# Optimization experiments

Hardware: AMD Instinct MI355X
Metric: run time of the kernel (lower is better)

The kernel has to match this reference:

```python
import jax, jax.numpy as jnp
import numpy as np

B, DIM, OC, H, W, HEADS = 4, 128, 128, 128, 128, 8
L = H * W
_BN_INV = 1.0 / (1.0 + 1e-5) ** 0.5  # eval-mode BN: running_mean=0, running_var=1


def conv2d(x, w, b=None, groups=1, pad=0):
    y = jax.lax.conv_general_dilated(
        x, w, (1, 1), [(pad, pad), (pad, pad)],
        dimension_numbers=('NCHW', 'OIHW', 'NCHW'),
        feature_group_count=groups)
    if b is not None:
        y = y + b[None, :, None, None]
    return y


def bn(x, g, b):
    return x * (g * _BN_INV)[None, :, None, None] + b[None, :, None, None]


def ln(x, g, b, eps=1e-5):
    m = jnp.mean(x, -1, keepdims=True)
    v = jnp.mean((x - m) ** 2, -1, keepdims=True)
    return (x - m) * jax.lax.rsqrt(v + eps) * g + b


def rope_tables(h, w, c, base=10000.0):
    k_max = c // 4
    theta = 1.0 / base ** (np.arange(k_max, dtype=np.float32) / k_max)
    gi, gj = np.meshgrid(np.arange(h, dtype=np.float32),
                         np.arange(w, dtype=np.float32), indexing='ij')
    ang = np.concatenate([gi[..., None] * theta, gj[..., None] * theta], -1)  # (h,w,c//2)
    return jnp.asarray(np.cos(ang)), jnp.asarray(np.sin(ang))


def apply_rope(x, cs, sn):  # x: (b,h,w,c); consecutive pairs = (re, im)
    xr, xi = x[..., 0::2], x[..., 1::2]
    return jnp.stack([cs * xr - sn * xi, sn * xr + cs * xi], -1).reshape(x.shape)


def linear_attn(x, qk_w, qk_b, lepe_w, lepe_b, h, w):
    b, n, c = x.shape
    hd = c // HEADS
    qk = x @ qk_w.T + qk_b
    q = jax.nn.elu(qk[..., :c]) + 1.0
    k = jax.nn.elu(qk[..., c:]) + 1.0
    cs, sn = rope_tables(h, w, c)

    def heads(t):  # (b,n,c) -> (b,HEADS,n,hd)
        return t.reshape(b, n, HEADS, hd).transpose(0, 2, 1, 3)

    q_r = heads(apply_rope(q.reshape(b, h, w, c), cs, sn).reshape(b, n, c))
    k_r = heads(apply_rope(k.reshape(b, h, w, c), cs, sn).reshape(b, n, c))
    qh, kh, vh = heads(q), heads(k), heads(x)
    k_mean = jnp.mean(kh, axis=2, keepdims=True)                      # (b,Hd,1,hd)
    z = 1.0 / (jnp.einsum('bhnd,bhmd->bhnm', qh, k_mean) + 1e-6)      # (b,Hd,n,1)
    s = n ** -0.5
    kv = jnp.einsum('bhnd,bhne->bhde', k_r * s, vh * s)               # (b,Hd,hd,hd)
    out = jnp.einsum('bhnd,bhde->bhne', q_r, kv) * z
    out = out.transpose(0, 2, 1, 3).reshape(b, n, c)
    v_img = x.reshape(b, h, w, c).transpose(0, 3, 1, 2)
    lepe = conv2d(v_img, lepe_w, lepe_b, groups=c, pad=1)
    return out + lepe.transpose(0, 2, 3, 1).reshape(b, n, c)


def fmt_block(xb, fw1, fb1, f_g, f_be, fw2, fb2, n_g, n_be):
    t = jnp.fft.fft2(xb)                                              # (B,C,H,W) complex
    wgt = jax.nn.relu(bn(conv2d(t.real, fw1, fb1), f_g, f_be))
    wgt = jax.nn.sigmoid(conv2d(wgt, fw2, fb2))
    f = jnp.abs(jnp.fft.ifft2(wgt * t))
    f = jax.nn.relu(bn(f, n_g, n_be))
    return f.reshape(f.shape[0], f.shape[1], -1).transpose(0, 2, 1)   # (B,L,C)


def _forward(x, c1_w, c1_b, c1_g, c1_be, cpe1_w, cpe1_b,
             fw1, fb1, f_g, f_be, fw2, fb2, nbn_g, nbn_be,
             ln1_g, ln1_b, d3w1, d3b1, d3w2, d5w1, d5b1, d5w2,
             ap_w, ap_b, ip2_w, ip2_b, dwc2_w, dwc2_b,
             qk_w, qk_b, lepe_w, lepe_b, op_w, op_b,
             cpe2_w, cpe2_b, ln2_g, ln2_b,
             ffn_w1, ffn_b1, ffn_w2, ffn_b2, po_w,
             red_w, red_b, red_g, red_be):
    Bb, C, Hh, Ww = x.shape
    Ll = Hh * Ww
    to_img = lambda t: t.reshape(Bb, Hh, Ww, C).transpose(0, 3, 1, 2)   # (B,L,C)->(B,C,H,W)
    to_seq = lambda t: t.transpose(0, 2, 3, 1).reshape(Bb, Ll, -1)       # (B,C,H,W)->(B,L,C)

    x_0 = jax.nn.relu(bn(conv2d(x, c1_w, c1_b), c1_g, c1_be))           # (B,OC,H,W)
    xt = to_seq(x + conv2d(x, cpe1_w, cpe1_b, groups=C, pad=1))
    shortcut = xt
    fmt1 = fmt_block(to_img(xt), fw1, fb1, f_g, f_be, fw2, fb2, nbn_g, nbn_be)

    x_s = ln(xt, ln1_g, ln1_b)
    xs_img = to_img(x_s)
    x_s3 = conv2d(conv2d(xs_img, d3w1, d3b1), d3w2, None, groups=C // 2, pad=1)
    x_s5 = conv2d(conv2d(xs_img, d5w1, d5b1), d5w2, None, groups=C // 2, pad=2)
    act_res = jax.nn.silu(to_seq(conv2d(xs_img, ap_w, ap_b)))

    def branch(t):  # (B,C/2,H,W) -> (B,L,C/2)
        t = conv2d(t, ip2_w, ip2_b)
        t = jax.nn.silu(conv2d(t, dwc2_w, dwc2_b, groups=C // 2, pad=1))
        return to_seq(t)

    a3 = linear_attn(branch(x_s3), qk_w, qk_b, lepe_w, lepe_b, Hh, Ww)
    a5 = linear_attn(branch(x_s5), qk_w, qk_b, lepe_w, lepe_b, Hh, Ww)
    xs = jnp.concatenate([a3, a5], -1)
    xs = to_seq(conv2d(to_img(xs * act_res), op_w, op_b))

    xt = shortcut + xs + fmt1
    xt = xt + to_seq(conv2d(to_img(xt), cpe2_w, cpe2_b, groups=C, pad=1))
    fmt2 = fmt_block(to_img(xt), fw1, fb1, f_g, f_be, fw2, fb2, nbn_g, nbn_be)
    h2 = ln(xt, ln2_g, ln2_b)
    ffn = jax.nn.gelu(h2 @ ffn_w1.T + ffn_b1, approximate=False) @ ffn_w2.T + ffn_b2
    xt = xt + ffn + fmt2

    xo = conv2d(to_img(xt), po_w)                                        # (B,OC,H,W)
    cat = jnp.concatenate([x_0, xo], 1)
    return jax.nn.relu(bn(conv2d(cat, red_w, red_b), red_g, red_be)) + x_0


def setup_inputs():
    key = jax.random.key(0)
    it = iter(jax.random.split(key, 64))

    def w(shape, s=0.05):
        return jax.random.normal(next(it), shape, jnp.float32) * s

    d, oc = DIM, OC
    ones = lambda n: jnp.ones((n,), jnp.float32)
    zeros = lambda n: jnp.zeros((n,), jnp.float32)
    return {
        'x': jax.random.normal(next(it), (B, d, H, W), jnp.float32),
        'c1_w': w((oc, d, 1, 1)), 'c1_b': w((oc,), 0.01), 'c1_g': ones(oc), 'c1_be': zeros(oc),
        'cpe1_w': w((d, 1, 3, 3)), 'cpe1_b': w((d,), 0.01),
        'fw1': w((d // 16, d, 1, 1)), 'fb1': w((d // 16,), 0.01),
        'f_g': ones(d // 16), 'f_be': zeros(d // 16),
        'fw2': w((d, d // 16, 1, 1)), 'fb2': w((d,), 0.01),
        'nbn_g': ones(d), 'nbn_be': zeros(d),
        'ln1_g': ones(d), 'ln1_b': zeros(d),
        'd3w1': w((d, d, 1, 1)), 'd3b1': w((d,), 0.01), 'd3w2': w((d // 2, 2, 3, 3)),
        'd5w1': w((d, d, 1, 1)), 'd5b1': w((d,), 0.01), 'd5w2': w((d // 2, 2, 5, 5)),
        'ap_w': w((d, d, 1, 1)), 'ap_b': w((d,), 0.01),
        'ip2_w': w((d // 2, d // 2, 1, 1)), 'ip2_b': w((d // 2,), 0.01),
        'dwc2_w': w((d // 2, 1, 3, 3)), 'dwc2_b': w((d // 2,), 0.01),
        'qk_w': w((d, d // 2)), 'qk_b': w((d,), 0.01),
        'lepe_w': w((d // 2, 1, 3, 3)), 'lepe_b': w((d // 2,), 0.01),
        'op_w': w((d, d, 1, 1)), 'op_b': w((d,), 0.01),
        'cpe2_w': w((d, 1, 3, 3)), 'cpe2_b': w((d,), 0.01),
        'ln2_g': ones(d), 'ln2_b': zeros(d),
        'ffn_w1': w((4, d)), 'ffn_b1': w((4,), 0.01),
        'ffn_w2': w((d, 4)), 'ffn_b2': w((d,), 0.01),
        'po_w': w((oc, d, 1, 1)),
        'red_w': w((oc, 2 * oc, 1, 1)), 'red_b': w((oc,), 0.01),
        'red_g': ones(oc), 'red_be': zeros(oc),
    }


def reference(x, c1_w, c1_b, c1_g, c1_be, cpe1_w, cpe1_b,
              fw1, fb1, f_g, f_be, fw2, fb2, nbn_g, nbn_be,
              ln1_g, ln1_b, d3w1, d3b1, d3w2, d5w1, d5b1, d5w2,
              ap_w, ap_b, ip2_w, ip2_b, dwc2_w, dwc2_b,
              qk_w, qk_b, lepe_w, lepe_b, op_w, op_b,
              cpe2_w, cpe2_b, ln2_g, ln2_b,
              ffn_w1, ffn_b1, ffn_w2, ffn_b2, po_w,
              red_w, red_b, red_g, red_be):
    return _forward(x, c1_w, c1_b, c1_g, c1_be, cpe1_w, cpe1_b,
                    fw1, fb1, f_g, f_be, fw2, fb2, nbn_g, nbn_be,
                    ln1_g, ln1_b, d3w1, d3b1, d3w2, d5w1, d5b1, d5w2,
                    ap_w, ap_b, ip2_w, ip2_b, dwc2_w, dwc2_b,
                    qk_w, qk_b, lepe_w, lepe_b, op_w, op_b,
                    cpe2_w, cpe2_b, ln2_g, ln2_b,
                    ffn_w1, ffn_b1, ffn_w2, ffn_b2, po_w,
                    red_w, red_b, red_g, red_be)
```

## Files before the change

kernel.cpp:

```cpp
#include <hip/hip_runtime.h>
#include <math.h>

typedef unsigned short bf16_t;
typedef __attribute__((ext_vector_type(8))) short short8;
typedef __attribute__((ext_vector_type(4))) float f32x4;

#define B_ 4
#define C_ 128
#define H_ 128
#define W_ 128
#define L_ (H_*W_)
#define NS  ((size_t)B_*L_*C_)
#define NH  ((size_t)B_*L_*64)
#define NSP ((size_t)L_*C_)
#define PI_F 3.14159265358979323846f
#define BN_INV 0.9999950000374997f
#define THETA_SC 0.8304820237218406f
#define TOTW 157148
#define W16SHIFT 107548

__device__ __forceinline__ float ldf(bf16_t v){ return __uint_as_float(((unsigned)v)<<16); }
__device__ __forceinline__ bf16_t f2b(float f){
  unsigned u = __float_as_uint(f);
  u += 0x7fffu + ((u>>16)&1u);
  return (bf16_t)(u>>16);
}

#define WGSZ ((size_t)B_*8*L_)
#define ACCSZ 2304
#define CWSZ 157184
#define CW16SZF 78592
#define WSF (6*NS + 3*NH + WGSZ + ACCSZ + CWSZ + CW16SZF + 16)
__device__ float g_ws[WSF];

__global__ void k_probe(const bf16_t* __restrict__ xb, int* __restrict__ flag){
  __shared__ int vote;
  if (threadIdx.x == 0) vote = 0;
  __syncthreads();
  int bad = 0;
  for (int i = threadIdx.x; i < 2048; i += 256) {
    float v = ldf(xb[2*i]);
    if (!(fabsf(v) < 1e6f)) bad = 1;
  }
  if (bad) atomicOr(&vote, 1);
  __syncthreads();
  if (threadIdx.x == 0) *flag = vote;
}

struct P47 { const void* p[47]; };
__device__ __constant__ int c_wsz[47] = {
  16384,128,128,128,1152,128,1024,8,8,8,1024,128,128,128,128,128,
  16384,128,1152,16384,128,3200,16384,128,4096,64,576,64,8192,128,
  576,64,16384,128,1152,128,128,128,512,4,512,128,16384,32768,128,128,128};

__global__ __launch_bounds__(256) void k_cvt(P47 ps, const int* __restrict__ flagp,
                                             float* __restrict__ dst){
  int g = blockIdx.x*256 + threadIdx.x;
  if (g >= TOTW) return;
  int fl = *flagp;
  int idx = 0, off = g;
  while (off >= c_wsz[idx]) { off -= c_wsz[idx]; idx++; }
  const void* s = ps.p[idx];
  dst[g] = fl ? ((const float*)s)[off] : ldf(((const bf16_t*)s)[off]);
}

__global__ __launch_bounds__(256) void k_cvt16(const float* __restrict__ src, bf16_t* __restrict__ dst){
  int g = blockIdx.x*256 + threadIdx.x;
  if (g >= TOTW) return;
  dst[g + (g >= W16SHIFT ? 4 : 0)] = f2b(src[g]);
}

__global__ void k_zero(float* p, int n){
  int i = blockIdx.x*256 + threadIdx.x;
  if (i < n) p[i] = 0.f;
}

__device__ __forceinline__ void tw_fwd(int lane, float* tc, float* ts) {
  sincosf(-PI_F * (float)lane * (1.f/64.f), &ts[0], &tc[0]);
  int i = 1;
  #pragma unroll
  for (int m = 32; m >= 1; m >>= 1, i++) {
    int k = lane & (m-1);
    sincosf(-PI_F * (float)k / (float)m, &ts[i], &tc[i]);
  }
}
__device__ __forceinline__ void tw_inv(int lane, float* tc, float* ts) {
  int i = 0;
  #pragma unroll
  for (int m = 1; m <= 32; m <<= 1, i++) {
    int k = lane & (m-1);
    sincosf(PI_F * (float)k / (float)m, &ts[i], &tc[i]);
  }
  sincosf(PI_F * (float)lane * (1.f/64.f), &ts[6], &tc[6]);
}

__device__ __forceinline__ void fft128_fwd(float& lor, float& loi, float& hir, float& hii,
                                           int lane, const float* tc, const float* ts) {
  {
    float s = ts[0], c = tc[0];
    float ar = lor, ai = loi;
    float dr = ar - hir, di = ai - hii;
    lor = ar + hir; loi = ai + hii;
    hir = dr*c - di*s; hii = dr*s + di*c;
  }
  int i = 1;
  #pragma unroll
  for (int m = 32; m >= 1; m >>= 1, i++) {
    float s = ts[i], c = tc[i];
    bool up = (lane & m) != 0;
    {
      float orr = __shfl_xor(lor, m), oii = __shfl_xor(loi, m);
      float sr = lor + orr, si = loi + oii;
      float dr = orr - lor, di = oii - loi;
      float tr = dr*c - di*s, ti = dr*s + di*c;
      lor = up ? tr : sr; loi = up ? ti : si;
    }
    {
      float orr = __shfl_xor(hir, m), oii = __shfl_xor(hii, m);
      float sr = hir + orr, si = hii + oii;
      float dr = orr - hir, di = oii - hii;
      float tr = dr*c - di*s, ti = dr*s + di*c;
      hir = up ? tr : sr; hii = up ? ti : si;
    }
  }
}

__device__ __forceinline__ void fft128_inv(float& lor, float& loi, float& hir, float& hii,
                                           int lane, const float* tc, const float* ts) {
  int i = 0;
  #pragma unroll
  for (int m = 1; m <= 32; m <<= 1, i++) {
    float s = ts[i], c = tc[i];
    bool up = (lane & m) != 0;
    {
      float orr = __shfl_xor(lor, m), oii = __shfl_xor(loi, m);
      float qr = orr*c - oii*s, qi = orr*s + oii*c;
      float lo_r = lor + qr, lo_i = loi + qi;
      float mr = lor*c - loi*s, mi = lor*s + loi*c;
      float up_r = orr - mr, up_i = oii - mi;
      lor = up ? up_r : lo_r; loi = up ? up_i : lo_i;
    }
    {
      float orr = __shfl_xor(hir, m), oii = __shfl_xor(hii, m);
      float qr = orr*c - oii*s, qi = orr*s + oii*c;
      float lo_r = hir + qr, lo_i = hii + qi;
      float mr = hir*c - hii*s, mi = hir*s + hii*c;
      float up_r = orr - mr, up_i = oii - mi;
      hir = up ? up_r : lo_r; hii = up ? up_i : lo_i;
    }
  }
  {
    float s = ts[6], c = tc[6];
    float qr = hir*c - hii*s, qi = hir*s + hii*c;
    float pr = lor, pi = loi;
    lor = pr + qr; loi = pi + qi;
    hir = pr - qr; hii = pi - qi;
  }
}

__global__ __launch_bounds__(256) void k_fft_row_fwd_seq(
    const float* __restrict__ in, float* __restrict__ re, float* __restrict__ im) {
  __shared__ float T[64*130];
  int tid = threadIdx.x;
  int bid = blockIdx.x;
  int ch = (bid & 1) * 64;
  int h  = (bid >> 1) & 127;
  int b  = bid >> 8;
  const float* ip = in + ((size_t)b*L_ + (size_t)h*128)*128 + ch;
  #pragma unroll
  for (int it = 0; it < 8; it++) {
    int idx = it*256 + tid;
    int c4 = (idx & 15)*4, w = idx >> 4;
    float4 v = *(const float4*)(ip + (size_t)w*128 + c4);
    T[(c4+0)*130 + w] = v.x;
    T[(c4+1)*130 + w] = v.y;
    T[(c4+2)*130 + w] = v.z;
    T[(c4+3)*130 + w] = v.w;
  }
  __syncthreads();
  int lane = tid & 63, wv = tid >> 6;
  float tc[7], ts[7];
  tw_fwd(lane, tc, ts);
  size_t obase = (size_t)(b*128 + ch)*L_ + (size_t)h*128;
  for (int i = 0; i < 16; i++) {
    int cc = wv*16 + i;
    float lor = T[cc*130 + lane], loi = 0.f;
    float hir = T[cc*130 + 64 + lane], hii = 0.f;
    fft128_fwd(lor, loi, hir, hii, lane, tc, ts);
    size_t o = obase + (size_t)cc*L_;
    re[o + lane] = lor;      im[o + lane] = loi;
    re[o + lane + 64] = hir; im[o + lane + 64] = hii;
  }
}

__global__ __launch_bounds__(256) void k_fft_col_fwd(float* __restrict__ re, float* __restrict__ im) {
  __shared__ float Lre[128][33];
  __shared__ float Lim[128][33];
  int tid = threadIdx.x;
  size_t img = blockIdx.x >> 2;
  int w0 = (blockIdx.x & 3) * 32;
  float* rp = re + img * (size_t)L_ + w0;
  float* ip = im + img * (size_t)L_ + w0;
  for (int i = tid; i < 4096; i += 256) {
    int h = i >> 5, wl = i & 31;
    Lre[h][wl] = rp[(size_t)h*W_ + wl];
    Lim[h][wl] = ip[(size_t)h*W_ + wl];
  }
  __syncthreads();
  int lane = tid & 63, wv = tid >> 6;
  float tc[7], ts[7];
  tw_fwd(lane, tc, ts);
  for (int i = 0; i < 8; i++) {
    int col = wv*8 + i;
    float lor = Lre[lane][col], loi = Lim[lane][col];
    float hir = Lre[lane+64][col], hii = Lim[lane+64][col];
    fft128_fwd(lor, loi, hir, hii, lane, tc, ts);
    Lre[lane][col]=lor; Lim[lane][col]=loi;
    Lre[lane+64][col]=hir; Lim[lane+64][col]=hii;
  }
  __syncthreads();
  for (int i = tid; i < 4096; i += 256) {
    int h = i >> 5, wl = i & 31;
    rp[(size_t)h*W_ + wl] = Lre[h][wl];
    ip[(size_t)h*W_ + wl] = Lim[h][wl];
  }
}

__global__ __launch_bounds__(256) void k_fft_col_inv_scaled(
    float* __restrict__ re, float* __restrict__ im,
    const float* __restrict__ wg1, const float* __restrict__ fw2,
    const float* __restrict__ fb2) {
  __shared__ float Lre[128][33];
  __shared__ float Lim[128][33];
  __shared__ float w2r[8];
  int tid = threadIdx.x;
  size_t img = blockIdx.x >> 2;
  int c = (int)(img & 127);
  int b = (int)(img >> 7);
  int w0 = (blockIdx.x & 3) * 32;
  if (tid < 8) w2r[tid] = fw2[c*8 + tid];
  float b2 = fb2[c];
  float* rp = re + img * (size_t)L_ + w0;
  float* ip = im + img * (size_t)L_ + w0;
  const float* wgp = wg1 + (size_t)b*8*L_ + w0;
  __syncthreads();
  for (int i = tid; i < 4096; i += 256) {
    int h = i >> 5, wl = i & 31;
    size_t p = (size_t)h*W_ + wl;
    float a = b2;
    #pragma unroll
    for (int o = 0; o < 8; o++) a += w2r[o] * wgp[(size_t)o*L_ + p];
    float wgt = 1.f/(1.f+expf(-a));
    Lre[h][wl] = rp[p] * wgt;
    Lim[h][wl] = ip[p] * wgt;
  }
  __syncthreads();
  int lane = tid & 63, wv = tid >> 6;
  float tc[7], ts[7];
  tw_inv(lane, tc, ts);
  for (int i = 0; i < 8; i++) {
    int col = wv*8 + i;
    float lor = Lre[lane][col], loi = Lim[lane][col];
    float hir = Lre[lane+64][col], hii = Lim[lane+64][col];
    fft128_inv(lor, loi, hir, hii, lane, tc, ts);
    Lre[lane][col]=lor*(1.f/128.f); Lim[lane][col]=loi*(1.f/128.f);
    Lre[lane+64][col]=hir*(1.f/128.f); Lim[lane+64][col]=hii*(1.f/128.f);
  }
  __syncthreads();
  for (int i = tid; i < 4096; i += 256) {
    int h = i >> 5, wl = i & 31;
    rp[(size_t)h*W_ + wl] = Lre[h][wl];
    ip[(size_t)h*W_ + wl] = Lim[h][wl];
  }
}

__global__ __launch_bounds__(256) void k_fft_row_inv_abs_seq(
    const float* __restrict__ re, const float* __restrict__ im,
    const float* __restrict__ ng, const float* __restrict__ nbe,
    const float* __restrict__ add1, const float* __restrict__ add2,
    float* __restrict__ out) {
  __shared__ float T[64*130];
  int tid = threadIdx.x;
  int bid = blockIdx.x;
  int ch = (bid & 1) * 64;
  int h  = (bid >> 1) & 127;
  int b  = bid >> 8;
  int lane = tid & 63, wv = tid >> 6;
  float tc[7], ts[7];
  tw_inv(lane, tc, ts);
  size_t ibase = (size_t)(b*128 + ch)*L_ + (size_t)h*128;
  for (int i = 0; i < 16; i++) {
    int cc = wv*16 + i;
    size_t o = ibase + (size_t)cc*L_;
    float lor = re[o + lane], loi = im[o + lane];
    float hir = re[o + lane + 64], hii = im[o + lane + 64];
    fft128_inv(lor, loi, hir, hii, lane, tc, ts);
    float sg = ng[ch+cc]*BN_INV, sb = nbe[ch+cc];
    T[cc*130 + lane]      = fmaxf(sqrtf(lor*lor+loi*loi)*(1.f/128.f)*sg + sb, 0.f);
    T[cc*130 + 64 + lane] = fmaxf(sqrtf(hir*hir+hii*hii)*(1.f/128.f)*sg + sb, 0.f);
  }
  __syncthreads();
  size_t sb0 = ((size_t)b*L_ + (size_t)h*128)*128 + ch;
  #pragma unroll
  for (int it = 0; it < 8; it++) {
    int idx = it*256 + tid;
    int c4 = (idx & 15)*4, w = idx >> 4;
    size_t off = sb0 + (size_t)w*128 + c4;
    float4 v;
    v.x = T[(c4+0)*130 + w];
    v.y = T[(c4+1)*130 + w];
    v.z = T[(c4+2)*130 + w];
    v.w = T[(c4+3)*130 + w];
    float4 x1 = *(const float4*)(add1 + off);
    float4 x2 = *(const float4*)(add2 + off);
    v.x += x1.x + x2.x; v.y += x1.y + x2.y;
    v.z += x1.z + x2.z; v.w += x1.w + x2.w;
    *(float4*)(out + off) = v;
  }
}

__global__ __launch_bounds__(256) void k_freq1(const float* __restrict__ tre,
    const float* __restrict__ fw1, const float* __restrict__ fb1,
    const float* __restrict__ fg, const float* __restrict__ fbe,
    float* __restrict__ wg1) {
  __shared__ float w1s[1024];
  int tid = threadIdx.x;
  for (int i = tid; i < 1024; i += 256) w1s[i] = fw1[i];
  __syncthreads();
  size_t g = (size_t)blockIdx.x*256 + tid;
  int p = (int)(g & (L_-1));
  int b = (int)(g >> 14);
  const float* tp = tre + (size_t)b*128*L_ + p;
  float acc[8];
  #pragma unroll
  for (int o = 0; o < 8; o++) acc[o] = 0.f;
  for (int c = 0; c < 128; c++) {
    float v = tp[(size_t)c*L_];
    #pragma unroll
    for (int o = 0; o < 8; o++) acc[o] += w1s[o*128+c]*v;
  }
  size_t ob = (size_t)b*8*L_ + p;
  #pragma unroll
  for (int o = 0; o < 8; o++) {
    float v = (acc[o] + fb1[o]) * (fg[o]*BN_INV) + fbe[o];
    wg1[ob + (size_t)o*L_] = fmaxf(v, 0.f);
  }
}

template<bool DUAL>
__global__ void k_p2s(const void* __restrict__ src, float* __restrict__ dst,
                      const float* __restrict__ add1, const float* __restrict__ add2,
                      const int* __restrict__ flagp) {
  __shared__ float tile[32][33];
  int fl = DUAL ? *flagp : 1;
  int b = blockIdx.z;
  int p0 = blockIdx.x*32, c0 = blockIdx.y*32;
  int tx = threadIdx.x, ty = threadIdx.y;
  size_t base_in = (size_t)b*NSP;
  #pragma unroll
  for (int k = 0; k < 4; k++) {
    size_t off = base_in + (size_t)(c0+ty+8*k)*L_ + p0 + tx;
    float v;
    if (DUAL && !fl) v = ldf(((const bf16_t*)src)[off]);
    else             v = ((const float*)src)[off];
    tile[ty+8*k][tx] = v;
  }
  __syncthreads();
  size_t base = (size_t)b*NSP;
  #pragma unroll
  for (int k = 0; k < 4; k++) {
    size_t idx = base + (size_t)(p0+ty+8*k)*C_ + c0 + tx;
    float v = tile[tx][ty+8*k];
    if (add1) v += add1[idx];
    if (add2) v += add2[idx];
    dst[idx] = v;
  }
}

template<int CC, int MODE>
__global__ __launch_bounds__(256) void k_dw3(const float* __restrict__ in,
    const float* __restrict__ w, const float* __restrict__ bias,
    float* __restrict__ out) {
  __shared__ float wl[9*CC];
  int tid = threadIdx.x;
  for (int i = tid; i < 9*CC; i += 256) {
    int tap = i / CC, ch = i % CC;
    wl[i] = w[ch*9 + tap];
  }
  __syncthreads();
  size_t g = (size_t)blockIdx.x*256 + tid;
  int c = (int)(g & (CC-1));
  float wr[9];
  #pragma unroll
  for (int t = 0; t < 9; t++) wr[t] = wl[t*CC + c];
  size_t s = g / CC;
  int w0 = (int)(s & 31) * 4;
  int hp = (int)((s >> 5) & 127);
  int b  = (int)(s >> 12);
  const float* ip = in + (size_t)b*L_*CC + c;
  float bi = bias[c];
  float a0 = bi, a1 = bi, a2 = bi, a3 = bi;
  #pragma unroll
  for (int dh = -1; dh <= 1; dh++) {
    int h2 = hp + dh;
    if ((unsigned)h2 >= 128u) continue;
    const float* rp = ip + (size_t)h2*W_*CC;
    float px[6];
    #pragma unroll
    for (int x = 0; x < 6; x++) {
      int w2 = w0 - 1 + x;
      px[x] = ((unsigned)w2 < 128u) ? rp[(size_t)w2*CC] : 0.f;
    }
    #pragma unroll
    for (int dw = 0; dw < 3; dw++) {
      float f = wr[(dh+1)*3 + dw];
      a0 += f*px[dw];   a1 += f*px[dw+1];
      a2 += f*px[dw+2]; a3 += f*px[dw+3];
    }
  }
  size_t tb = (size_t)b*L_ + (size_t)hp*W_ + w0;
  if (MODE == 0) {
    out[(tb+0)*CC + c] = in[(tb+0)*CC + c] + a0;
    out[(tb+1)*CC + c] = in[(tb+1)*CC + c] + a1;
    out[(tb+2)*CC + c] = in[(tb+2)*CC + c] + a2;
    out[(tb+3)*CC + c] = in[(tb+3)*CC + c] + a3;
  } else {
    out[(tb+0)*CC + c] = a0 / (1.f + expf(-a0));
    out[(tb+1)*CC + c] = a1 / (1.f + expf(-a1));
    out[(tb+2)*CC + c] = a2 / (1.f + expf(-a2));
    out[(tb+3)*CC + c] = a3 / (1.f + expf(-a3));
  }
}

template<int K>
__global__ __launch_bounds__(256) void k_gconv(const float* __restrict__ in,
    const float* __restrict__ w, float* __restrict__ out) {
  __shared__ float wl[K*K*128];
  int tid = threadIdx.x;
  for (int i = tid; i < 128*K*K; i += 256) {
    int tap = i >> 7, ch = i & 127;
    wl[i] = w[ch*(K*K) + tap];
  }
  __syncthreads();
  size_t g = (size_t)blockIdx.x*256 + tid;
  int oc = (int)(g & 63);
  float wx[K*K], wy[K*K];
  #pragma unroll
  for (int t = 0; t < K*K; t++) {
    wx[t] = wl[t*128 + 2*oc];
    wy[t] = wl[t*128 + 2*oc + 1];
  }
  size_t s = g >> 6;
  int w0 = (int)(s & 31) * 4;
  int hp = (int)((s >> 5) & 127);
  int b  = (int)(s >> 12);
  const float* ip = in + (size_t)b*L_*128 + 2*oc;
  constexpr int P = K/2;
  float a0 = 0.f, a1 = 0.f, a2 = 0.f, a3 = 0.f;
  #pragma unroll
  for (int kh = 0; kh < K; kh++) {
    int h2 = hp + kh - P;
    if ((unsigned)h2 >= 128u) continue;
    const float* rp = ip + (size_t)h2*W_*128;
    float2 px[K+3];
    #pragma unroll
    for (int x = 0; x < K+3; x++) {
      int w2 = w0 - P + x;
      px[x] = ((unsigned)w2 < 128u) ? *(const float2*)(rp + (size_t)w2*128)
                                    : make_float2(0.f, 0.f);
    }
    #pragma unroll
    for (int kw = 0; kw < K; kw++) {
      float fx = wx[kh*K + kw], fy = wy[kh*K + kw];
      a0 += fx*px[kw+0].x + fy*px[kw+0].y;
      a1 += fx*px[kw+1].x + fy*px[kw+1].y;
      a2 += fx*px[kw+2].x + fy*px[kw+2].y;
      a3 += fx*px[kw+3].x + fy*px[kw+3].y;
    }
  }
  size_t tb = (size_t)b*L_ + (size_t)hp*W_ + w0;
  out[(tb+0)*64 + oc] = a0;
  out[(tb+1)*64 + oc] = a1;
  out[(tb+2)*64 + oc] = a2;
  out[(tb+3)*64 + oc] = a3;
}

template<int CIN, int COUT, int EPI, bool MUL>
__global__ __launch_bounds__(256) void k_mfma_tok(
    const float* __restrict__ in, const float* __restrict__ mulp,
    const bf16_t* __restrict__ W16, const float* __restrict__ bias,
    float* __restrict__ out) {
  constexpr int NO = COUT/16;
  int tid = threadIdx.x;
  int lane = tid & 63, wv = tid >> 6;
  int m = lane & 15, q = lane >> 4;
  size_t t0 = (size_t)blockIdx.x*64 + (size_t)wv*16;
  f32x4 acc[NO];
  #pragma unroll
  for (int i = 0; i < NO; i++) acc[i] = (f32x4){0.f,0.f,0.f,0.f};
  for (int k0 = 0; k0 < CIN; k0 += 32) {
    const float* ap = in + (t0 + m)*CIN + k0 + q*8;
    float4 a0 = *(const float4*)ap;
    float4 a1 = *(const float4*)(ap + 4);
    if (MUL) {
      const float* mp = mulp + (t0 + m)*CIN + k0 + q*8;
      float4 m0 = *(const float4*)mp;
      float4 m1 = *(const float4*)(mp + 4);
      a0.x*=m0.x; a0.y*=m0.y; a0.z*=m0.z; a0.w*=m0.w;
      a1.x*=m1.x; a1.y*=m1.y; a1.z*=m1.z; a1.w*=m1.w;
    }
    union { short s[8]; short8 v; } af;
    af.s[0]=(short)f2b(a0.x); af.s[1]=(short)f2b(a0.y);
    af.s[2]=(short)f2b(a0.z); af.s[3]=(short)f2b(a0.w);
    af.s[4]=(short)f2b(a1.x); af.s[5]=(short)f2b(a1.y);
    af.s[6]=(short)f2b(a1.z); af.s[7]=(short)f2b(a1.w);
    #pragma unroll
    for (int o = 0; o < NO; o++) {
      short8 bf = *(const short8*)(W16 + (size_t)(o*16 + m)*CIN + k0 + q*8);
      acc[o] = __builtin_amdgcn_mfma_f32_16x16x32_bf16(af.v, bf, acc[o], 0, 0, 0);
    }
  }
  #pragma unroll
  for (int o = 0; o < NO; o++) {
    float bv = (EPI >= 1) ? bias[o*16 + m] : 0.f;
    #pragma unroll
    for (int r = 0; r < 4; r++) {
      int row = q*4 + r;
      float v = acc[o][r] + bv;
      if (EPI == 2) v = v / (1.f + expf(-v));
      if (EPI == 3) v = v > 0.f ? v + 1.f : expf(v);
      out[(t0 + row)*COUT + o*16 + m] = v;
    }
  }
}

__global__ __launch_bounds__(256) void k_mfma_c1(
    const float* __restrict__ in, const bf16_t* __restrict__ W16,
    const float* __restrict__ bias, const float* __restrict__ gam,
    const float* __restrict__ bet, float* __restrict__ out) {
  constexpr int NO = 8;
  int tid = threadIdx.x;
  int lane = tid & 63, wv = tid >> 6;
  int m = lane & 15, q = lane >> 4;
  size_t t0 = (size_t)blockIdx.x*64 + (size_t)wv*16;
  f32x4 acc[NO];
  #pragma unroll
  for (int i = 0; i < NO; i++) acc[i] = (f32x4){0.f,0.f,0.f,0.f};
  for (int k0 = 0; k0 < 128; k0 += 32) {
    const float* ap = in + (t0 + m)*128 + k0 + q*8;
    float4 a0 = *(const float4*)ap;
    float4 a1 = *(const float4*)(ap + 4);
    union { short s[8]; short8 v; } af;
    af.s[0]=(short)f2b(a0.x); af.s[1]=(short)f2b(a0.y);
    af.s[2]=(short)f2b(a0.z); af.s[3]=(short)f2b(a0.w);
    af.s[4]=(short)f2b(a1.x); af.s[5]=(short)f2b(a1.y);
    af.s[6]=(short)f2b(a1.z); af.s[7]=(short)f2b(a1.w);
    #pragma unroll
    for (int o = 0; o < NO; o++) {
      short8 bf = *(const short8*)(W16 + (size_t)(o*16 + m)*128 + k0 + q*8);
      acc[o] = __builtin_amdgcn_mfma_f32_16x16x32_bf16(af.v, bf, acc[o], 0, 0, 0);
    }
  }
  #pragma unroll
  for (int o = 0; o < NO; o++) {
    int oc = o*16 + m;
    float bi = bias[oc], gm = gam[oc]*BN_INV, be = bet[oc];
    #pragma unroll
    for (int r = 0; r < 4; r++) {
      int row = q*4 + r;
      float v = acc[o][r] + bi;
      out[(t0 + row)*128 + oc] = fmaxf(v*gm + be, 0.f);
    }
  }
}

__global__ __launch_bounds__(256) void k_mfma_red(
    const float* __restrict__ x0s, const float* __restrict__ xo,
    const bf16_t* __restrict__ W16, const float* __restrict__ bias,
    const float* __restrict__ gam, const float* __restrict__ bet,
    void* __restrict__ out, const int* __restrict__ flagp) {
  __shared__ float T[128*65];
  constexpr int NO = 8;
  int fl = *flagp;
  int tid = threadIdx.x;
  int lane = tid & 63, wv = tid >> 6;
  int m = lane & 15, q = lane >> 4;
  size_t t0 = (size_t)blockIdx.x*64;
  size_t tw = t0 + (size_t)wv*16;
  f32x4 acc[NO];
  #pragma unroll
  for (int i = 0; i < NO; i++) acc[i] = (f32x4){0.f,0.f,0.f,0.f};
  for (int k0 = 0; k0 < 256; k0 += 32) {
    const float* src = (k0 < 128) ? (x0s + (tw + m)*128 + k0)
                                  : (xo  + (tw + m)*128 + (k0 - 128));
    float4 a0 = *(const float4*)(src + q*8);
    float4 a1 = *(const float4*)(src + q*8 + 4);
    union { short s[8]; short8 v; } af;
    af.s[0]=(short)f2b(a0.x); af.s[1]=(short)f2b(a0.y);
    af.s[2]=(short)f2b(a0.z); af.s[3]=(short)f2b(a0.w);
    af.s[4]=(short)f2b(a1.x); af.s[5]=(short)f2b(a1.y);
    af.s[6]=(short)f2b(a1.z); af.s[7]=(short)f2b(a1.w);
    #pragma unroll
    for (int o = 0; o < NO; o++) {
      short8 bf = *(const short8*)(W16 + (size_t)(o*16 + m)*256 + k0 + q*8);
      acc[o] = __builtin_amdgcn_mfma_f32_16x16x32_bf16(af.v, bf, acc[o], 0, 0, 0);
    }
  }
  #pragma unroll
  for (int ot = 0; ot < NO; ot++) {
    int o = ot*16 + m;
    float bi = bias[o], gm = gam[o]*BN_INV, be = bet[o];
    #pragma unroll
    for (int r = 0; r < 4; r++) {
      int row = q*4 + r;
      float v = acc[ot][r] + bi;
      v = fmaxf(v*gm + be, 0.f);
      v += x0s[(tw + row)*128 + o];
      T[o*65 + wv*16 + row] = v;
    }
  }
  __syncthreads();
  int b = (int)(t0 >> 14);
  int p0 = (int)(t0 & (L_-1));
  if (!fl) {
    bf16_t* op = (bf16_t*)out;
    for (int i = tid; i < 8192; i += 256) {
      int o = i >> 6, tk = i & 63;
      op[((size_t)b*128 + o)*L_ + p0 + tk] = f2b(T[o*65 + tk]);
    }
  } else {
    float* op = (float*)out;
    for (int i = tid; i < 8192; i += 256) {
      int o = i >> 6, tk = i & 63;
      op[((size_t)b*128 + o)*L_ + p0 + tk] = T[o*65 + tk];
    }
  }
}

__global__ __launch_bounds__(256) void k_ln(const float* __restrict__ in,
    const float* __restrict__ g, const float* __restrict__ be, float* __restrict__ out) {
  int tid = threadIdx.x, lane = tid & 63;
  size_t t = (size_t)blockIdx.x*4 + (tid >> 6);
  const float* row = in + t*128;
  float2 v = *(const float2*)(row + lane*2);
  float s = v.x + v.y, ss = v.x*v.x + v.y*v.y;
  #pragma unroll
  for (int m = 1; m < 64; m <<= 1) { s += __shfl_xor(s, m); ss += __shfl_xor(ss, m); }
  float mean = s*(1.f/128.f);
  float inv = rsqrtf(ss*(1.f/128.f) - mean*mean + 1e-5f);
  float2 o;
  o.x = (v.x-mean)*inv*g[lane*2]   + be[lane*2];
  o.y = (v.y-mean)*inv*g[lane*2+1] + be[lane*2+1];
  *(float2*)(out + t*128 + lane*2) = o;
}

__global__ __launch_bounds__(256) void k_ln_ffn(const float* __restrict__ in,
    const float* __restrict__ g, const float* __restrict__ be,
    const float* __restrict__ w1, const float* __restrict__ b1,
    const float* __restrict__ w2, const float* __restrict__ b2,
    float* __restrict__ out) {
  int tid = threadIdx.x, lane = tid & 63;
  size_t t = (size_t)blockIdx.x*4 + (tid >> 6);
  const float* row = in + t*128;
  float2 v = *(const float2*)(row + lane*2);
  float s = v.x + v.y, ss = v.x*v.x + v.y*v.y;
  #pragma unroll
  for (int m = 1; m < 64; m <<= 1) { s += __shfl_xor(s, m); ss += __shfl_xor(ss, m); }
  float mean = s*(1.f/128.f);
  float inv = rsqrtf(ss*(1.f/128.f) - mean*mean + 1e-5f);
  float hx = (v.x-mean)*inv*g[lane*2]   + be[lane*2];
  float hy = (v.y-mean)*inv*g[lane*2+1] + be[lane*2+1];
  float hp0 = hx*w1[0*128+lane*2] + hy*w1[0*128+lane*2+1];
  float hp1 = hx*w1[1*128+lane*2] + hy*w1[1*128+lane*2+1];
  float hp2 = hx*w1[2*128+lane*2] + hy*w1[2*128+lane*2+1];
  float hp3 = hx*w1[3*128+lane*2] + hy*w1[3*128+lane*2+1];
  #pragma unroll
  for (int m = 1; m < 64; m <<= 1) {
    hp0 += __shfl_xor(hp0, m); hp1 += __shfl_xor(hp1, m);
    hp2 += __shfl_xor(hp2, m); hp3 += __shfl_xor(hp3, m);
  }
  float hv0, hv1, hv2, hv3;
  { float a = hp0 + b1[0]; hv0 = 0.5f*a*(1.f+erff(a*0.7071067811865476f)); }
  { float a = hp1 + b1[1]; hv1 = 0.5f*a*(1.f+erff(a*0.7071067811865476f)); }
  { float a = hp2 + b1[2]; hv2 = 0.5f*a*(1.f+erff(a*0.7071067811865476f)); }
  { float a = hp3 + b1[3]; hv3 = 0.5f*a*(1.f+erff(a*0.7071067811865476f)); }
  int cx = lane*2, cy = lane*2+1;
  float2 o;
  o.x = hv0*w2[cx*4+0] + hv1*w2[cx*4+1] + hv2*w2[cx*4+2] + hv3*w2[cx*4+3] + b2[cx];
  o.y = hv0*w2[cy*4+0] + hv1*w2[cy*4+1] + hv2*w2[cy*4+2] + hv3*w2[cy*4+3] + b2[cy];
  *(float2*)(out + t*128 + lane*2) = o;
}

__global__ __launch_bounds__(256) void k_kv(
    const float* __restrict__ qk, const float* __restrict__ v,
    float* __restrict__ akv_g, float* __restrict__ aks_g) {
  __shared__ float kvred[512];
  __shared__ float ksred[64];
  int tid = threadIdx.x;
  for (int i = tid; i < 512; i += 256) kvred[i] = 0.f;
  if (tid < 64) ksred[tid] = 0.f;
  __syncthreads();
  int lane = tid & 63, wv = tid >> 6;
  size_t t0 = (size_t)blockIdx.x * 64;
  int b = (int)(t0 >> 14);
  int pr = lane >> 1;
  float theta = exp2f(-(float)(pr & 15) * THETA_SC);
  bool use_i = pr < 16;
  int hbase = lane & 56;
  float akv[8];
  #pragma unroll
  for (int d = 0; d < 8; d++) akv[d] = 0.f;
  float aks = 0.f;
  for (int it = 0; it < 16; it++) {
    size_t t = t0 + (size_t)wv*16 + it;
    float k = qk[t*128 + 64 + lane];
    float xv = v[t*64 + lane];
    int l = (int)(t & (L_-1));
    float pos = use_i ? (float)(l >> 7) : (float)(l & 127);
    float sn, cs; sincosf(pos*theta, &sn, &cs);
    float kp = __shfl_xor(k, 1);
    float kr = (lane & 1) ? (sn*kp + cs*k) : (cs*k - sn*kp);
    #pragma unroll
    for (int d = 0; d < 8; d++) {
      float krd = __shfl(kr, hbase + d);
      akv[d] += krd * xv;
    }
    aks += k;
  }
  int h8 = lane >> 3, e = lane & 7;
  #pragma unroll
  for (int d = 0; d < 8; d++)
    atomicAdd(&kvred[h8*64 + d*8 + e], akv[d]);
  atomicAdd(&ksred[lane], aks);
  __syncthreads();
  for (int i = tid; i < 512; i += 256) atomicAdd(&akv_g[b*512 + i], kvred[i]);
  if (tid < 64) atomicAdd(&aks_g[b*64 + tid], ksred[tid]);
}

__global__ __launch_bounds__(256) void k_attn2(
    const float* __restrict__ qk, const float* __restrict__ x,
    const float* __restrict__ akv_g, const float* __restrict__ aks_g,
    const float* __restrict__ lw, const float* __restrict__ lb,
    float* __restrict__ out, int coff) {
  __shared__ float kv[512];
  __shared__ float km[64];
  __shared__ float lwl[576];
  int tid = threadIdx.x;
  size_t t0 = (size_t)blockIdx.x * 32;
  int b = (int)(t0 >> 14);
  const float invn = 1.f/16384.f;
  for (int i = tid; i < 512; i += 256) kv[i] = akv_g[b*512 + i]*invn;
  if (tid < 64) km[tid] = aks_g[b*64 + tid]*invn;
  for (int i = tid; i < 576; i += 256) lwl[i] = lw[i];
  __syncthreads();
  int lane = tid & 63, wv = tid >> 6;
  int pr = lane >> 1;
  float theta = exp2f(-(float)(pr & 15) * THETA_SC);
  bool use_i = pr < 16;
  int hbase = lane & 56, e = lane & 7;
  float lbv = lb[lane];
  const float* xb = x + ((size_t)b << 14) * 64;
  for (int it = 0; it < 8; it++) {
    size_t t = t0 + (size_t)wv*8 + it;
    int l = (int)(t & (L_-1));
    int ipos = l >> 7, jpos = l & 127;
    float q = qk[t*128 + lane];
    float p = q * km[lane];
    p += __shfl_xor(p, 1); p += __shfl_xor(p, 2); p += __shfl_xor(p, 4);
    float z = 1.f/(p + 1e-6f);
    float pos = use_i ? (float)ipos : (float)jpos;
    float sn, cs; sincosf(pos*theta, &sn, &cs);
    float qp = __shfl_xor(q, 1);
    float qr = (lane & 1) ? (sn*qp + cs*q) : (cs*q - sn*qp);
    float acc = 0.f;
    #pragma unroll
    for (int d = 0; d < 8; d++) {
      float qrd = __shfl(qr, hbase + d);
      acc += qrd * kv[hbase*8 + d*8 + e];
    }
    acc *= z;
    float lp = lbv;
    #pragma unroll
    for (int dh = -1; dh <= 1; dh++) {
      int h2 = ipos + dh; if ((unsigned)h2 >= 128u) continue;
      #pragma unroll
      for (int dw = -1; dw <= 1; dw++) {
        int w2 = jpos + dw; if ((unsigned)w2 >= 128u) continue;
        lp += lwl[lane*9 + (dh+1)*3 + (dw+1)] * xb[((size_t)(h2 << 7) + w2)*64 + lane];
      }
    }
    out[t*128 + coff + lane] = acc + lp;
  }
}

extern "C" void kernel_launch(void* const* d_in, const int* in_sizes, int n_in,
                              void* d_out, int out_size, void* d_ws, size_t ws_size,
                              hipStream_t stream) {
  (void)in_sizes; (void)n_in; (void)out_size;

  float* base;
  if (ws_size >= WSF * sizeof(float)) {
    base = (float*)d_ws;
  } else {
    void* p = nullptr;
    hipGetSymbolAddress(&p, HIP_SYMBOL(g_ws));
    base = (float*)p;
  }
  float* P0 = base;
  float* PA = base + 1*NS;
  float* PB = base + 2*NS;
  float* PC = base + 3*NS;
  float* PD = base + 4*NS;
  float* PF = base + 5*NS;
  float* H0 = base + 6*NS;
  float* H1 = H0 + NH;
  float* H2 = H1 + NH;
  float* WG = H2 + NH;
  float* ACC = WG + WGSZ;
  float* CW  = ACC + ACCSZ;
  bf16_t* CW16 = (bf16_t*)(CW + CWSZ);
  int*   FLG = (int*)(CW + CWSZ + CW16SZF);

  static const int wsz[47] = {
    16384,128,128,128,1152,128,1024,8,8,8,1024,128,128,128,128,128,
    16384,128,1152,16384,128,3200,16384,128,4096,64,576,64,8192,128,
    576,64,16384,128,1152,128,128,128,512,4,512,128,16384,32768,128,128,128};
  int woff[47]; { int a = 0; for (int i = 0; i < 47; i++){ woff[i] = a; a += wsz[i]; } }
  const float* Wf[47]; for (int i = 0; i < 47; i++) Wf[i] = CW + woff[i];
  auto W16 = [&](int i){ return (const bf16_t*)(CW16 + woff[i] + (woff[i] >= W16SHIFT ? 4 : 0)); };
  const float *c1_b=Wf[1], *c1_g=Wf[2], *c1_be=Wf[3], *cpe1_w=Wf[4],
    *cpe1_b=Wf[5], *fw1=Wf[6], *fb1=Wf[7], *f_g=Wf[8], *f_be=Wf[9], *fw2=Wf[10],
    *fb2=Wf[11], *nbn_g=Wf[12], *nbn_be=Wf[13], *ln1_g=Wf[14], *ln1_b=Wf[15],
    *d3b1=Wf[17], *d3w2=Wf[18], *d5b1=Wf[20],
    *d5w2=Wf[21], *ap_b=Wf[23], *ip2_b=Wf[25],
    *dwc2_w=Wf[26], *dwc2_b=Wf[27], *qk_b=Wf[29], *lepe_w=Wf[30],
    *lepe_b=Wf[31], *op_b=Wf[33], *cpe2_w=Wf[34], *cpe2_b=Wf[35],
    *ln2_g=Wf[36], *ln2_b=Wf[37], *ffn_w1=Wf[38], *ffn_b1=Wf[39], *ffn_w2=Wf[40],
    *ffn_b2=Wf[41], *red_b=Wf[44], *red_g=Wf[45], *red_be=Wf[46];
  const bf16_t *c1_w16=W16(0), *d3w1_16=W16(16), *d5w1_16=W16(19), *ap_w16=W16(22),
    *ip2_w16=W16(24), *qk_w16=W16(28), *op_w16=W16(32), *po_w16=W16(42), *red_w16=W16(43);

  const void* x = d_in[0];

  k_probe<<<1, 256, 0, stream>>>((const bf16_t*)x, FLG);
  P47 ps; for (int i = 0; i < 47; i++) ps.p[i] = d_in[i+1];
  k_cvt<<<(TOTW+255)/256, 256, 0, stream>>>(ps, FLG, CW);
  k_cvt16<<<(TOTW+255)/256, 256, 0, stream>>>(CW, CW16);

  dim3 tgrid(512, 4, 4), tblk(32, 8);

  auto fmt_fused = [&](const float* seq_in, float* re, float* im,
                       const float* add1, const float* add2, float* outp) {
    k_fft_row_fwd_seq<<<1024, 256, 0, stream>>>(seq_in, re, im);
    k_fft_col_fwd<<<2048, 256, 0, stream>>>(re, im);
    k_freq1<<<256, 256, 0, stream>>>(re, fw1, fb1, f_g, f_be, WG);
    k_fft_col_inv_scaled<<<2048, 256, 0, stream>>>(re, im, WG, fw2, fb2);
    k_fft_row_inv_abs_seq<<<1024, 256, 0, stream>>>(re, im, nbn_g, nbn_be, add1, add2, outp);
  };

  auto attn = [&](const float* brin, float* qkbuf, int coff) {
    k_zero<<<9, 256, 0, stream>>>(ACC, 2304);
    k_mfma_tok<64,128,3,false><<<1024, 256, 0, stream>>>(brin, nullptr, qk_w16, qk_b, qkbuf);
    k_kv<<<1024, 256, 0, stream>>>(qkbuf, brin, ACC, ACC + B_*512);
    k_attn2<<<2048, 256, 0, stream>>>(qkbuf, brin, ACC, ACC + B_*512, lepe_w, lepe_b, PF, coff);
  };

  k_p2s<true><<<tgrid, tblk, 0, stream>>>(x, PA, nullptr, nullptr, FLG);
  k_mfma_c1<<<1024, 256, 0, stream>>>(PA, c1_w16, c1_b, c1_g, c1_be, P0);
  k_dw3<128,0><<<8192, 256, 0, stream>>>(PA, cpe1_w, cpe1_b, PB);
  k_ln<<<16384, 256, 0, stream>>>(PB, ln1_g, ln1_b, PA);
  k_mfma_tok<128,128,1,false><<<1024, 256, 0, stream>>>(PA, nullptr, d3w1_16, d3b1, PD);
  k_gconv<3><<<4096, 256, 0, stream>>>(PD, d3w2, H0);
  k_mfma_tok<128,128,1,false><<<1024, 256, 0, stream>>>(PA, nullptr, d5w1_16, d5b1, PD);
  k_gconv<5><<<4096, 256, 0, stream>>>(PD, d5w2, H1);
  k_mfma_tok<128,128,2,false><<<1024, 256, 0, stream>>>(PA, nullptr, ap_w16, ap_b, PA);
  k_mfma_tok<64,64,1,false><<<1024, 256, 0, stream>>>(H0, nullptr, ip2_w16, ip2_b, H2);
  k_dw3<64,1><<<4096, 256, 0, stream>>>(H2, dwc2_w, dwc2_b, H0);
  attn(H0, PD, 0);
  k_mfma_tok<64,64,1,false><<<1024, 256, 0, stream>>>(H1, nullptr, ip2_w16, ip2_b, H2);
  k_dw3<64,1><<<4096, 256, 0, stream>>>(H2, dwc2_w, dwc2_b, H1);
  attn(H1, PD, 64);
  k_mfma_tok<128,128,1,true><<<1024, 256, 0, stream>>>(PF, PA, op_w16, op_b, PF);
  fmt_fused(PB, PC, PD, PB, PF, PB);
  k_dw3<128,0><<<8192, 256, 0, stream>>>(PB, cpe2_w, cpe2_b, PC);
  k_ln_ffn<<<16384, 256, 0, stream>>>(PC, ln2_g, ln2_b, ffn_w1, ffn_b1, ffn_w2, ffn_b2, PF);
  fmt_fused(PC, PB, PD, PC, PF, PC);
  k_mfma_tok<128,128,0,false><<<1024, 256, 0, stream>>>(PC, nullptr, po_w16, nullptr, PD);
  k_mfma_red<<<1024, 256, 0, stream>>>(P0, PD, red_w16, red_b, red_g, red_be, d_out, FLG);
}
```

Before: 1.003 ms.

## Use real-input FFT symmetry to halve frequency-domain storage and work

The forward row FFT now packs two real channels into one complex 128-point FFT and splits them using Hermitian symmetry, storing only 65 (padded to 66) frequency bins per row. The column FFTs, frequency gating, and sigmoid scaling operate on the half spectrum. The inverse row pass rebuilds the full spectrum from two channels' half spectra and recovers both real outputs from one complex inverse FFT. The aim is to roughly halve FFT arithmetic and the intermediate memory traffic in the frequency block, at the cost of more shuffles and more complex indexing. It also assumes the per-bin gating keeps the spectrum Hermitian.

New measurement: 975.4 us. 1.03x faster.

```diff
diff --git a/kernel.cpp b/kernel.cpp
--- a/kernel.cpp
+++ b/kernel.cpp
@@ -19,6 +19,9 @@
 #define TOTW 157148
 #define W16SHIFT 107548
 
+#define W2_ 66
+#define L2_ (128*W2_)
+
 __device__ __forceinline__ float ldf(bf16_t v){ return __uint_as_float(((unsigned)v)<<16); }
 __device__ __forceinline__ bf16_t f2b(float f){
   unsigned u = __float_as_uint(f);
@@ -26,11 +29,12 @@
   return (bf16_t)(u>>16);
 }
 
-#define WGSZ ((size_t)B_*8*L_)
+#define WGSZ ((size_t)B_*8*L2_)
+#define WGSLOT ((size_t)B_*8*L_)
 #define ACCSZ 2304
 #define CWSZ 157184
 #define CW16SZF 78592
-#define WSF (6*NS + 3*NH + WGSZ + ACCSZ + CWSZ + CW16SZF + 16)
+#define WSF (6*NS + 3*NH + WGSLOT + ACCSZ + CWSZ + CW16SZF + 16)
 __device__ float g_ws[WSF];
 
 __global__ void k_probe(const bf16_t* __restrict__ xb, int* __restrict__ flag){
@@ -158,7 +162,7 @@
   }
 }
 
-__global__ __launch_bounds__(256) void k_fft_row_fwd_seq(
+__global__ __launch_bounds__(256) void k_fft_row_fwd_half(
     const float* __restrict__ in, float* __restrict__ re, float* __restrict__ im) {
   __shared__ float T[64*130];
   int tid = threadIdx.x;
@@ -179,39 +183,55 @@
   }
   __syncthreads();
   int lane = tid & 63, wv = tid >> 6;
+  int rb = (int)(__brev((unsigned)lane) >> 26);
+  int pe = (64 - lane) & 63;
+  int po = 63 - lane;
   float tc[7], ts[7];
   tw_fwd(lane, tc, ts);
-  size_t obase = (size_t)(b*128 + ch)*L_ + (size_t)h*128;
-  for (int i = 0; i < 16; i++) {
-    int cc = wv*16 + i;
-    float lor = T[cc*130 + lane], loi = 0.f;
-    float hir = T[cc*130 + 64 + lane], hii = 0.f;
+  #pragma unroll
+  for (int t = 0; t < 8; t++) {
+    int ca = wv*16 + 2*t, cb = ca + 1;
+    float lor = T[ca*130 + lane],      loi = T[cb*130 + lane];
+    float hir = T[ca*130 + 64 + lane], hii = T[cb*130 + 64 + lane];
     fft128_fwd(lor, loi, hir, hii, lane, tc, ts);
-    size_t o = obase + (size_t)cc*L_;
-    re[o + lane] = lor;      im[o + lane] = loi;
-    re[o + lane + 64] = hir; im[o + lane + 64] = hii;
-  }
-}
-
-__global__ __launch_bounds__(256) void k_fft_col_fwd(float* __restrict__ re, float* __restrict__ im) {
-  __shared__ float Lre[128][33];
-  __shared__ float Lim[128][33];
-  int tid = threadIdx.x;
-  size_t img = blockIdx.x >> 2;
-  int w0 = (blockIdx.x & 3) * 32;
-  float* rp = re + img * (size_t)L_ + w0;
-  float* ip = im + img * (size_t)L_ + w0;
-  for (int i = tid; i < 4096; i += 256) {
-    int h = i >> 5, wl = i & 31;
-    Lre[h][wl] = rp[(size_t)h*W_ + wl];
-    Lim[h][wl] = ip[(size_t)h*W_ + wl];
+    float er  = __shfl(lor, rb), ei  = __shfl(loi, rb);
+    float our = __shfl(hir, rb), oui = __shfl(hii, rb);
+    float per = __shfl(er, pe),  pei = __shfl(ei, pe);
+    float por = __shfl(our, po), poi = __shfl(oui, po);
+    float ae_r = 0.5f*(er + per),  ae_i = 0.5f*(ei - pei);
+    float be_r = 0.5f*(ei + pei),  be_i = 0.5f*(per - er);
+    float ao_r = 0.5f*(our + por), ao_i = 0.5f*(oui - poi);
+    float bo_r = 0.5f*(oui + poi), bo_i = 0.5f*(por - our);
+    if (lane == 32) { ao_r = 0.f; ao_i = 0.f; bo_r = 0.f; bo_i = 0.f; }
+    if (lane <= 32) {
+      size_t ba = (size_t)(b*128 + ch + ca)*L2_ + (size_t)h*W2_ + 2*lane;
+      size_t bb = (size_t)(b*128 + ch + cb)*L2_ + (size_t)h*W2_ + 2*lane;
+      *(float2*)(re + ba) = make_float2(ae_r, ao_r);
+      *(float2*)(im + ba) = make_float2(ae_i, ao_i);
+      *(float2*)(re + bb) = make_float2(be_r, bo_r);
+      *(float2*)(im + bb) = make_float2(be_i, bo_i);
+    }
+  }
+}
+
+__global__ __launch_bounds__(256) void k_fft_col_fwd_h(float* __restrict__ re, float* __restrict__ im) {
+  __shared__ float Lre[128][34];
+  __shared__ float Lim[128][34];
+  int tid = threadIdx.x;
+  size_t img = blockIdx.x >> 1;
+  int w0 = (blockIdx.x & 1) * 33;
+  float* rp = re + img * (size_t)L2_ + w0;
+  float* ip = im + img * (size_t)L2_ + w0;
+  for (int i = tid; i < 4224; i += 256) {
+    int h = i / 33, wl = i - h*33;
+    Lre[h][wl] = rp[(size_t)h*W2_ + wl];
+    Lim[h][wl] = ip[(size_t)h*W2_ + wl];
   }
   __syncthreads();
   int lane = tid & 63, wv = tid >> 6;
   float tc[7], ts[7];
   tw_fwd(lane, tc, ts);
-  for (int i = 0; i < 8; i++) {
-    int col = wv*8 + i;
+  for (int col = wv; col < 33; col += 4) {
     float lor = Lre[lane][col], loi = Lim[lane][col];
     float hir = Lre[lane+64][col], hii = Lim[lane+64][col];
     fft128_fwd(lor, loi, hir, hii, lane, tc, ts);
@@ -219,37 +239,37 @@
     Lre[lane+64][col]=hir; Lim[lane+64][col]=hii;
   }
   __syncthreads();
-  for (int i = tid; i < 4096; i += 256) {
-    int h = i >> 5, wl = i & 31;
-    rp[(size_t)h*W_ + wl] = Lre[h][wl];
-    ip[(size_t)h*W_ + wl] = Lim[h][wl];
-  }
-}
-
-__global__ __launch_bounds__(256) void k_fft_col_inv_scaled(
+  for (int i = tid; i < 4224; i += 256) {
+    int h = i / 33, wl = i - h*33;
+    rp[(size_t)h*W2_ + wl] = Lre[h][wl];
+    ip[(size_t)h*W2_ + wl] = Lim[h][wl];
+  }
+}
+
+__global__ __launch_bounds__(256) void k_fft_col_inv_scaled_h(
     float* __restrict__ re, float* __restrict__ im,
     const float* __restrict__ wg1, const float* __restrict__ fw2,
     const float* __restrict__ fb2) {
-  __shared__ float Lre[128][33];
-  __shared__ float Lim[128][33];
+  __shared__ float Lre[128][34];
+  __shared__ float Lim[128][34];
   __shared__ float w2r[8];
   int tid = threadIdx.x;
-  size_t img = blockIdx.x >> 2;
+  size_t img = blockIdx.x >> 1;
   int c = (int)(img & 127);
   int b = (int)(img >> 7);
-  int w0 = (blockIdx.x & 3) * 32;
+  int w0 = (blockIdx.x & 1) * 33;
   if (tid < 8) w2r[tid] = fw2[c*8 + tid];
   float b2 = fb2[c];
-  float* rp = re + img * (size_t)L_ + w0;
-  float* ip = im + img * (size_t)L_ + w0;
-  const float* wgp = wg1 + (size_t)b*8*L_ + w0;
-  __syncthreads();
-  for (int i = tid; i < 4096; i += 256) {
-    int h = i >> 5, wl = i & 31;
-    size_t p = (size_t)h*W_ + wl;
+  float* rp = re + img * (size_t)L2_ + w0;
+  float* ip = im + img * (size_t)L2_ + w0;
+  const float* wgp = wg1 + (size_t)b*8*L2_ + w0;
+  __syncthreads();
+  for (int i = tid; i < 4224; i += 256) {
+    int h = i / 33, wl = i - h*33;
+    size_t p = (size_t)h*W2_ + wl;
     float a = b2;
     #pragma unroll
-    for (int o = 0; o < 8; o++) a += w2r[o] * wgp[(size_t)o*L_ + p];
+    for (int o = 0; o < 8; o++) a += w2r[o] * wgp[(size_t)o*L2_ + p];
     float wgt = 1.f/(1.f+expf(-a));
     Lre[h][wl] = rp[p] * wgt;
     Lim[h][wl] = ip[p] * wgt;
@@ -258,8 +278,7 @@
   int lane = tid & 63, wv = tid >> 6;
   float tc[7], ts[7];
   tw_inv(lane, tc, ts);
-  for (int i = 0; i < 8; i++) {
-    int col = wv*8 + i;
+  for (int col = wv; col < 33; col += 4) {
     float lor = Lre[lane][col], loi = Lim[lane][col];
     float hir = Lre[lane+64][col], hii = Lim[lane+64][col];
     fft128_inv(lor, loi, hir, hii, lane, tc, ts);
@@ -267,37 +286,79 @@
     Lre[lane+64][col]=hir*(1.f/128.f); Lim[lane+64][col]=hii*(1.f/128.f);
   }
   __syncthreads();
-  for (int i = tid; i < 4096; i += 256) {
-    int h = i >> 5, wl = i & 31;
-    rp[(size_t)h*W_ + wl] = Lre[h][wl];
-    ip[(size_t)h*W_ + wl] = Lim[h][wl];
-  }
-}
-
-__global__ __launch_bounds__(256) void k_fft_row_inv_abs_seq(
+  for (int i = tid; i < 4224; i += 256) {
+    int h = i / 33, wl = i - h*33;
+    rp[(size_t)h*W2_ + wl] = Lre[h][wl];
+    ip[(size_t)h*W2_ + wl] = Lim[h][wl];
+  }
+}
+
+__global__ __launch_bounds__(256) void k_fft_row_inv_abs_seq_h(
     const float* __restrict__ re, const float* __restrict__ im,
     const float* __restrict__ ng, const float* __restrict__ nbe,
     const float* __restrict__ add1, const float* __restrict__ add2,
     float* __restrict__ out) {
-  __shared__ float T[64*130];
+  __shared__ float S[64*132];
   int tid = threadIdx.x;
   int bid = blockIdx.x;
   int ch = (bid & 1) * 64;
   int h  = (bid >> 1) & 127;
   int b  = bid >> 8;
+  {
+    const float* rbase = re + (size_t)(b*128 + ch)*L2_ + (size_t)h*W2_;
+    const float* ibase = im + (size_t)(b*128 + ch)*L2_ + (size_t)h*W2_;
+    for (int i = tid; i < 64*66; i += 256) {
+      int c = i / 66, v = i - c*66;
+      S[c*132 + v]      = rbase[(size_t)c*L2_ + v];
+      S[c*132 + 66 + v] = ibase[(size_t)c*L2_ + v];
+    }
+  }
+  __syncthreads();
   int lane = tid & 63, wv = tid >> 6;
+  int rb = (int)(__brev((unsigned)lane) >> 26);
+  int vlo = 2*rb, vhi = vlo + 1;
   float tc[7], ts[7];
   tw_inv(lane, tc, ts);
-  size_t ibase = (size_t)(b*128 + ch)*L_ + (size_t)h*128;
-  for (int i = 0; i < 16; i++) {
-    int cc = wv*16 + i;
-    size_t o = ibase + (size_t)cc*L_;
-    float lor = re[o + lane], loi = im[o + lane];
-    float hir = re[o + lane + 64], hii = im[o + lane + 64];
+  float rr[8][4];
+  #pragma unroll
+  for (int t = 0; t < 8; t++) {
+    int ca = wv*16 + 2*t, cb = ca + 1;
+    const float* Sa = S + ca*132;
+    const float* Sb = S + cb*132;
+    float lor, loi, hir, hii;
+    if (vlo <= 64) {
+      float ar = Sa[vlo], ai = Sa[66+vlo], br = Sb[vlo], bi = Sb[66+vlo];
+      lor = ar - bi; loi = ai + br;
+    } else {
+      int u = 128 - vlo;
+      float ar = Sa[u], ai = Sa[66+u], br = Sb[u], bi = Sb[66+u];
+      lor = ar + bi; loi = br - ai;
+    }
+    if (vhi <= 64) {
+      float ar = Sa[vhi], ai = Sa[66+vhi], br = Sb[vhi], bi = Sb[66+vhi];
+      hir = ar - bi; hii = ai + br;
+    } else {
+      int u = 128 - vhi;
+      float ar = Sa[u], ai = Sa[66+u], br = Sb[u], bi = Sb[66+u];
+      hir = ar + bi; hii = br - ai;
+    }
     fft128_inv(lor, loi, hir, hii, lane, tc, ts);
-    float sg = ng[ch+cc]*BN_INV, sb = nbe[ch+cc];
-    T[cc*130 + lane]      = fmaxf(sqrtf(lor*lor+loi*loi)*(1.f/128.f)*sg + sb, 0.f);
-    T[cc*130 + 64 + lane] = fmaxf(sqrtf(hir*hir+hii*hii)*(1.f/128.f)*sg + sb, 0.f);
+    rr[t][0] = fabsf(lor);
+    rr[t][1] = fabsf(loi);
+    rr[t][2] = fabsf(hir);
+    rr[t][3] = fabsf(hii);
+  }
+  __syncthreads();
+  float* T = S;
+  #pragma unroll
+  for (int t = 0; t < 8; t++) {
+    int ca = wv*16 + 2*t, cb = ca + 1;
+    float sga = ng[ch+ca]*BN_INV, sba = nbe[ch+ca];
+    float sgb = ng[ch+cb]*BN_INV, sbb = nbe[ch+cb];
+    T[ca*130 + lane]      = fmaxf(rr[t][0]*(1.f/128.f)*sga + sba, 0.f);
+    T[cb*130 + lane]      = fmaxf(rr[t][1]*(1.f/128.f)*sgb + sbb, 0.f);
+    T[ca*130 + 64 + lane] = fmaxf(rr[t][2]*(1.f/128.f)*sga + sba, 0.f);
+    T[cb*130 + 64 + lane] = fmaxf(rr[t][3]*(1.f/128.f)*sgb + sbb, 0.f);
   }
   __syncthreads();
   size_t sb0 = ((size_t)b*L_ + (size_t)h*128)*128 + ch;
@@ -319,7 +380,7 @@
   }
 }
 
-__global__ __launch_bounds__(256) void k_freq1(const float* __restrict__ tre,
+__global__ __launch_bounds__(256) void k_freq1_h(const float* __restrict__ tre,
     const float* __restrict__ fw1, const float* __restrict__ fb1,
     const float* __restrict__ fg, const float* __restrict__ fbe,
     float* __restrict__ wg1) {
@@ -328,22 +389,22 @@
   for (int i = tid; i < 1024; i += 256) w1s[i] = fw1[i];
   __syncthreads();
   size_t g = (size_t)blockIdx.x*256 + tid;
-  int p = (int)(g & (L_-1));
-  int b = (int)(g >> 14);
-  const float* tp = tre + (size_t)b*128*L_ + p;
+  int p = (int)(g % L2_);
+  int b = (int)(g / L2_);
+  const float* tp = tre + (size_t)b*128*L2_ + p;
   float acc[8];
   #pragma unroll
   for (int o = 0; o < 8; o++) acc[o] = 0.f;
   for (int c = 0; c < 128; c++) {
-    float v = tp[(size_t)c*L_];
+    float v = tp[(size_t)c*L2_];
     #pragma unroll
     for (int o = 0; o < 8; o++) acc[o] += w1s[o*128+c]*v;
   }
-  size_t ob = (size_t)b*8*L_ + p;
+  size_t ob = (size_t)b*8*L2_ + p;
   #pragma unroll
   for (int o = 0; o < 8; o++) {
     float v = (acc[o] + fb1[o]) * (fg[o]*BN_INV) + fbe[o];
-    wg1[ob + (size_t)o*L_] = fmaxf(v, 0.f);
+    wg1[ob + (size_t)o*L2_] = fmaxf(v, 0.f);
   }
 }
 
@@ -816,7 +877,7 @@
   float* H1 = H0 + NH;
   float* H2 = H1 + NH;
   float* WG = H2 + NH;
-  float* ACC = WG + WGSZ;
+  float* ACC = WG + WGSLOT;
   float* CW  = ACC + ACCSZ;
   bf16_t* CW16 = (bf16_t*)(CW + CWSZ);
   int*   FLG = (int*)(CW + CWSZ + CW16SZF);
@@ -851,11 +912,11 @@
 
   auto fmt_fused = [&](const float* seq_in, float* re, float* im,
                        const float* add1, const float* add2, float* outp) {
-    k_fft_row_fwd_seq<<<1024, 256, 0, stream>>>(seq_in, re, im);
-    k_fft_col_fwd<<<2048, 256, 0, stream>>>(re, im);
-    k_freq1<<<256, 256, 0, stream>>>(re, fw1, fb1, f_g, f_be, WG);
-    k_fft_col_inv_scaled<<<2048, 256, 0, stream>>>(re, im, WG, fw2, fb2);
-    k_fft_row_inv_abs_seq<<<1024, 256, 0, stream>>>(re, im, nbn_g, nbn_be, add1, add2, outp);
+    k_fft_row_fwd_half<<<1024, 256, 0, stream>>>(seq_in, re, im);
+    k_fft_col_fwd_h<<<1024, 256, 0, stream>>>(re, im);
+    k_freq1_h<<<132, 256, 0, stream>>>(re, fw1, fb1, f_g, f_be, WG);
+    k_fft_col_inv_scaled_h<<<1024, 256, 0, stream>>>(re, im, WG, fw2, fb2);
+    k_fft_row_inv_abs_seq_h<<<1024, 256, 0, stream>>>(re, im, nbn_g, nbn_be, add1, add2, outp);
   };
 
   auto attn = [&](const float* brin, float* qkbuf, int coff) {
```
